# Kernel tuning notes

Hardware: AMD Instinct MI355X
Metric: run time of the kernel (lower is better)

Reference implementation:

```python
import jax, jax.numpy as jnp
import numpy as np

N_QUBITS = 12          # hidden_features = number of wires
QDEPTH = 8             # StronglyEntanglingLayers depth
INPUT_DIM = 784        # c*w*h = 1*28*28
DIM = 2 ** N_QUBITS    # statevector size

# bit table: wire 0 = most significant bit (PennyLane convention)
_BITS = ((np.arange(DIM)[:, None] >> np.arange(N_QUBITS - 1, -1, -1)[None, :]) & 1)  # (DIM, N)
_ZVALS = (1.0 - 2.0 * _BITS).astype(np.float32)  # (DIM, N): eigvals of PauliZ per wire

def _cz_diag(r):
    # diagonal of the product of CZ(i, (i+r)%N) for i in range(N); duplicates cancel (CZ^2=I)
    d = np.ones(DIM, np.float32)
    for i in range(N_QUBITS):
        j = (i + r) % N_QUBITS
        d *= 1.0 - 2.0 * (_BITS[:, i] * _BITS[:, j]).astype(np.float32)
    return d

# per-layer CZ entangler diagonal; PennyLane default range r = l % (N-1) + 1
_CZ_DIAGS = [jnp.asarray(_cz_diag((l % (N_QUBITS - 1)) + 1)) for l in range(QDEPTH)]


def _apply_rot(state, w3, wire):
    # Rot(phi, theta, omega) = RZ(omega) RY(theta) RZ(phi) applied to one wire
    phi, theta, omega = w3[0], w3[1], w3[2]
    c = jnp.cos(theta / 2).astype(jnp.complex64)
    s = jnp.sin(theta / 2).astype(jnp.complex64)
    m00 = jnp.exp(-0.5j * (phi + omega)) * c
    m01 = -jnp.exp(0.5j * (phi - omega)) * s
    m10 = jnp.exp(-0.5j * (phi - omega)) * s
    m11 = jnp.exp(0.5j * (phi + omega)) * c
    M = jnp.stack([jnp.stack([m00, m01]), jnp.stack([m10, m11])])  # (2,2) complex64
    b = state.shape[0]
    st = state.reshape(b, 2 ** wire, 2, -1)
    st = jnp.einsum('pq,bkqr->bkpr', M, st)
    return st.reshape(b, DIM)


def _quantum_layer(angles, qweights):
    # angles: (b, N) RZ-encoded inputs; qweights: (QDEPTH, N, 3)
    b = angles.shape[0]
    # initial |0...0>; RZ(angle_j) on |0> contributes phase exp(-i*angle_j/2)
    amp0 = jnp.exp(-0.5j * jnp.sum(angles, axis=1))  # (b,) complex64
    state = jnp.zeros((b, DIM), jnp.complex64).at[:, 0].set(amp0)
    for l in range(QDEPTH):
        for j in range(N_QUBITS):
            state = _apply_rot(state, qweights[l, j], j)
        state = state * _CZ_DIAGS[l][None, :]
    probs = state.real ** 2 + state.imag ** 2  # (b, DIM)
    return probs @ jnp.asarray(_ZVALS)         # (b, N) <Z_i> expvals


def setup_inputs() -> dict:
    key = jax.random.key(0)
    ks = jax.random.split(key, 6)
    b = 2048
    x = jax.random.normal(ks[0], (b, 1, 28, 28), jnp.float32)
    sd = 1.0 / np.sqrt(INPUT_DIM)
    su = 1.0 / np.sqrt(N_QUBITS)
    w_down = jax.random.normal(ks[1], (N_QUBITS, INPUT_DIM), jnp.float32) * sd
    b_down = jax.random.normal(ks[2], (N_QUBITS,), jnp.float32) * sd
    w_up = jax.random.normal(ks[3], (INPUT_DIM, N_QUBITS), jnp.float32) * su
    b_up = jax.random.normal(ks[4], (INPUT_DIM,), jnp.float32) * su
    qweights = jax.random.normal(ks[5], (QDEPTH, N_QUBITS, 3), jnp.float32) * 0.4
    return {"x": x, "w_down": w_down, "b_down": b_down, "w_up": w_up, "b_up": b_up, "qweights": qweights}


def reference(x, w_down, b_down, w_up, b_up, qweights):
    b, c, w, h = x.shape
    xf = x.reshape(b, -1)
    x_reduced = xf @ w_down.T + b_down            # (b, N_QUBITS)
    z = _quantum_layer(x_reduced, qweights)       # (b, N_QUBITS)
    x_restored = z @ w_up.T + b_up                # (b, INPUT_DIM)
    return x_restored.reshape(b, c, w, h)
```

## Files before the change

kernel.cpp:

```cpp
#include <hip/hip_runtime.h>

#define NQ     12
#define DIM    4096
#define QDEPTH 8
#define T      1024
#define NBLK   256

typedef _Float16 h2 __attribute__((ext_vector_type(2)));
union S4 { float4 f; h2 h[4]; };
union HB { h2 h; unsigned u; int i; };

__device__ __forceinline__ int SW(int i) {
    return i ^ ((i >> 6) & 0xF) ^ (((i >> 10) & 1) << 4);
}

template <int CTRL>
__device__ __forceinline__ int dpp_i(int x) {
    return __builtin_amdgcn_update_dpp(x, x, CTRL, 0xF, 0xF, false);
}
template <int CTRL>
__device__ __forceinline__ float dpp_mov(float x) {
    return __int_as_float(dpp_i<CTRL>(__float_as_int(x)));
}
__device__ __forceinline__ float swz_xor4f(float x) {
    return __int_as_float(__builtin_amdgcn_ds_swizzle(__float_as_int(x), 0x101F));
}

template <int KIND>
__device__ __forceinline__ h2 xlane(h2 x) {
    HB b; b.h = x;
    if constexpr (KIND == 0)      b.i = dpp_i<0xB1>(b.i);
    else if constexpr (KIND == 1) b.i = dpp_i<0x4E>(b.i);
    else if constexpr (KIND == 2) b.i = __builtin_amdgcn_ds_swizzle(b.i, 0x101F);
    else                          b.i = dpp_i<0x128>(b.i);
    return b.h;
}

__device__ __forceinline__ h2 csw(h2 a) { return __builtin_shufflevector(a, a, 1, 0); }
__device__ __forceinline__ h2 cmul(h2 rr, h2 ii, h2 a) { return rr * a + ii * csw(a); }
__device__ __forceinline__ h2 cfma(h2 rr, h2 ii, h2 a, h2 acc) { return acc + rr * a + ii * csw(a); }

__device__ __forceinline__ void reg_gate(h2 a[4], const int m, const S4 S0, const S4 S1) {
#pragma unroll
    for (int c = 0; c < 4; ++c) {
        if (c & m) continue;
        const int c1 = c | m;
        const h2 a0 = a[c], a1 = a[c1];
        h2 n0 = cmul(S0.h[0], S0.h[1], a0); n0 = cfma(S0.h[2], S0.h[3], a1, n0);
        h2 n1 = cmul(S1.h[2], S1.h[3], a0); n1 = cfma(S1.h[0], S1.h[1], a1, n1);
        a[c] = n0; a[c1] = n1;
    }
}

template <int KIND>
__device__ __forceinline__ void lane_gate(h2 a[4], const S4 C) {
#pragma unroll
    for (int c = 0; c < 4; ++c) {
        const h2 p = xlane<KIND>(a[c]);
        h2 n = cmul(C.h[0], C.h[1], a[c]);
        a[c] = cfma(C.h[2], C.h[3], p, n);
    }
}

__device__ __forceinline__ void load_coefs(const float4* __restrict__ m4,
                                           const int gi0, const int lane, S4 R[8]) {
    const float4* G = m4 + gi0 * 2;
    R[0].f = G[0]; R[1].f = G[1]; R[2].f = G[2]; R[3].f = G[3];
    R[4].f = G[4  + ((lane >> 3) & 1)];
    R[5].f = G[6  + ((lane >> 2) & 1)];
    R[6].f = G[8  + ((lane >> 1) & 1)];
    R[7].f = G[10 + ( lane       & 1)];
}

__device__ __forceinline__ void apply6(h2 a[4], const S4 R[8]) {
    reg_gate(a, 2, R[0], R[1]);
    reg_gate(a, 1, R[2], R[3]);
    lane_gate<3>(a, R[4]);
    lane_gate<2>(a, R[5]);
    lane_gate<1>(a, R[6]);
    lane_gate<0>(a, R[7]);
}

__device__ __forceinline__ void apply_cz(h2 a[4], const int ii[4], const int d) {
    const int r = d + 1;
#pragma unroll
    for (int c = 0; c < 4; ++c) {
        const unsigned i  = (unsigned)ii[c];
        const unsigned ro = ((i << r) | (i >> (12 - r))) & 0xFFFu;
        HB b; b.h = a[c];
        b.u ^= (__popc(i & ro) & 1) ? 0x80008000u : 0u;
        a[c] = b.h;
    }
}

__device__ __forceinline__ void merged_pass(h2* __restrict__ st,
                                            const float4* __restrict__ m4,
                                            const int ja[4], const int ii[4],
                                            const int gbase, const int l1,
                                            const int lane, h2 a[4]) {
    S4 R1[8], R2[8];
    load_coefs(m4, l1 * NQ + gbase, lane, R1);
    __syncthreads();
#pragma unroll
    for (int c = 0; c < 4; ++c) a[c] = st[ja[c]];
    load_coefs(m4, (l1 + 1) * NQ + gbase, lane, R2);
    apply6(a, R1);
    apply_cz(a, ii, l1);
    apply6(a, R2);
#pragma unroll
    for (int c = 0; c < 4; ++c) st[ja[c]] = a[c];
}

__global__ __launch_bounds__(T) void qnn_fused(const float* __restrict__ qw,
                                               const float* __restrict__ w_up,
                                               const float* __restrict__ b_up,
                                               float* __restrict__ out) {
    __shared__ h2     st[DIM];
    __shared__ float4 mats4[96 * 2];
    __shared__ float  zred[T / 64][NQ];
    __shared__ float  zfin[NQ];
    __shared__ float4 row4[196];

    const int tid  = threadIdx.x;
    const int lane = tid & 63;

    if (tid < 192) {
        const int g = tid >> 1, hh = tid & 1;
        const float phi = qw[g * 3 + 0], theta = qw[g * 3 + 1], omega = qw[g * 3 + 2];
        float c, s, sp, cp, sm, cm;
        sincosf(0.5f * theta, &s, &c);
        sincosf(0.5f * (phi + omega), &sp, &cp);
        sincosf(0.5f * (phi - omega), &sm, &cm);
        S4 u;
        if (hh == 0) {
            u.h[0] = (h2){(_Float16)(cp * c),  (_Float16)(cp * c)};
            u.h[1] = (h2){(_Float16)(sp * c),  (_Float16)(-sp * c)};
            u.h[2] = (h2){(_Float16)(-cm * s), (_Float16)(-cm * s)};
            u.h[3] = (h2){(_Float16)(sm * s),  (_Float16)(-sm * s)};
        } else {
            u.h[0] = (h2){(_Float16)(cp * c),  (_Float16)(cp * c)};
            u.h[1] = (h2){(_Float16)(-sp * c), (_Float16)(sp * c)};
            u.h[2] = (h2){(_Float16)(cm * s),  (_Float16)(cm * s)};
            u.h[3] = (h2){(_Float16)(sm * s),  (_Float16)(-sm * s)};
        }
        mats4[g * 2 + hh] = u.f;
    }
    __syncthreads();

    const int w4 = (tid >> 6) & 0xF, l54 = (tid >> 4) & 3, l30 = tid & 0xF;
    int jaA[4], iiA[4], jaB[4], iiB[4];
#pragma unroll
    for (int c = 0; c < 4; ++c) {
        iiA[c] = (c << 10) | (l30 << 6) | (l54 << 4) | w4;
        iiB[c] = (l54 << 10) | (w4 << 6) | (c << 4) | l30;
        jaA[c] = SW(iiA[c]);
        jaB[c] = SW(iiB[c]);
    }

    h2 a[4];
    {
        S4 R1[8], R2[8];
        load_coefs(mats4, 0 * NQ + 6, lane, R1);
        load_coefs(mats4, 1 * NQ + 6, lane, R2);
        const int h = (l54 << 4) | w4;
        float pr = 1.f, pi = 0.f;
#pragma unroll
        for (int k = 0; k < 6; ++k) {
            const int b = (h >> (5 - k)) & 1;
            S4 u; u.f = mats4[k * 2 + b];
            const float cr = (float)(b ? u.h[2].x : u.h[0].x);
            const float ci = (float)(b ? u.h[3].y : u.h[1].y);
            const float nr = pr * cr - pi * ci;
            const float ni = pr * ci + pi * cr;
            pr = nr; pi = ni;
        }
        a[0] = (l30 == 0) ? (h2){(_Float16)pr, (_Float16)pi}
                          : (h2){(_Float16)0.f, (_Float16)0.f};
        a[1] = a[2] = a[3] = (h2){(_Float16)0.f, (_Float16)0.f};
        apply6(a, R1);
        apply_cz(a, iiB, 0);
        apply6(a, R2);
#pragma unroll
        for (int c = 0; c < 4; ++c) st[jaB[c]] = a[c];
    }
    merged_pass(st, mats4, jaA, iiA, 0, 1, lane, a);
    merged_pass(st, mats4, jaB, iiB, 6, 2, lane, a);
    merged_pass(st, mats4, jaA, iiA, 0, 3, lane, a);
    merged_pass(st, mats4, jaB, iiB, 6, 4, lane, a);
    merged_pass(st, mats4, jaA, iiA, 0, 5, lane, a);
    merged_pass(st, mats4, jaB, iiB, 6, 6, lane, a);
    {
        S4 R1[8];
        load_coefs(mats4, 7 * NQ + 0, lane, R1);
        __syncthreads();
#pragma unroll
        for (int c = 0; c < 4; ++c) a[c] = st[jaA[c]];
        apply6(a, R1);
    }

    float p4[4];
#pragma unroll
    for (int c = 0; c < 4; ++c) {
        const float ar = (float)a[c].x, ai = (float)a[c].y;
        p4[c] = ar * ar + ai * ai;
    }
    const float s01 = p4[0] + p4[1], s23 = p4[2] + p4[3];
    const float S = s01 + s23;
    float zp[NQ];
    zp[0] = s01 - s23;
    zp[1] = (p4[0] - p4[1]) + (p4[2] - p4[3]);
#pragma unroll
    for (int w = 2; w < NQ; ++w)
        zp[w] = (((iiA[0] >> (11 - w)) & 1) ? -S : S);

#pragma unroll
    for (int w = 0; w < NQ; ++w) {
        float v = zp[w];
        v += dpp_mov<0xB1>(v);
        v += dpp_mov<0x4E>(v);
        v += swz_xor4f(v);
        v += dpp_mov<0x128>(v);
        const float r0 = __int_as_float(__builtin_amdgcn_readlane(__float_as_int(v), 0));
        const float r1 = __int_as_float(__builtin_amdgcn_readlane(__float_as_int(v), 16));
        const float r2 = __int_as_float(__builtin_amdgcn_readlane(__float_as_int(v), 32));
        const float r3 = __int_as_float(__builtin_amdgcn_readlane(__float_as_int(v), 48));
        zp[w] = (r0 + r1) + (r2 + r3);
    }
    const int wave = tid >> 6;
    if (lane == 0) {
#pragma unroll
        for (int w = 0; w < NQ; ++w) zred[wave][w] = zp[w];
    }
    __syncthreads();
    if (tid < NQ) {
        float v = 0.0f;
#pragma unroll
        for (int k = 0; k < T / 64; ++k) v += zred[k][tid];
        zfin[tid] = v;
    }
    __syncthreads();

    if (tid < 784) {
        float acc = b_up[tid];
#pragma unroll
        for (int j = 0; j < NQ; ++j) acc += zfin[j] * w_up[tid * NQ + j];
        ((float*)row4)[tid] = acc;
    }
    __syncthreads();

    if (tid < 784) {
        const float4 v = row4[tid % 196];
        float4* o = (float4*)out;
        const int base = blockIdx.x * 1568;
        o[base + tid]       = v;
        o[base + 784 + tid] = v;
    }
}

extern "C" void kernel_launch(void* const* d_in, const int* in_sizes, int n_in,
                              void* d_out, int out_size, void* d_ws, size_t ws_size,
                              hipStream_t stream) {
    const float* w_up = (const float*)d_in[3];
    const float* b_up = (const float*)d_in[4];
    const float* qw   = (const float*)d_in[5];
    float* out = (float*)d_out;

    qnn_fused<<<NBLK, T, 0, stream>>>(qw, w_up, b_up, out);
}
```

Baseline: 84.77 us.

## Halve block size and process eight amplitudes per thread

Cuts the block from 1024 to 512 threads, so each thread holds 8 statevector amplitudes instead of 4. Three qubits are now handled by in-register gates, which removes the ds_swizzle cross-lane gate and leaves three DPP lane gates. The index mapping and the LDS swizzle are rewritten for the new layout, and the output loops become strided. The aim is to cut cross-lane and barrier overhead per amplitude and raise per-thread ILP, at the cost of more registers per thread and fewer waves to hide latency.

```diff
diff --git a/kernel.cpp b/kernel.cpp
--- a/kernel.cpp
+++ b/kernel.cpp
@@ -3,7 +3,7 @@
 #define NQ     12
 #define DIM    4096
 #define QDEPTH 8
-#define T      1024
+#define T      512
 #define NBLK   256
 
 typedef _Float16 h2 __attribute__((ext_vector_type(2)));
@@ -11,7 +11,7 @@
 union HB { h2 h; unsigned u; int i; };
 
 __device__ __forceinline__ int SW(int i) {
-    return i ^ ((i >> 6) & 0xF) ^ (((i >> 10) & 1) << 4);
+    return i ^ ((i >> 5) & 7) ^ (((i >> 9) & 3) << 3);
 }
 
 template <int CTRL>
@@ -31,7 +31,6 @@
     HB b; b.h = x;
     if constexpr (KIND == 0)      b.i = dpp_i<0xB1>(b.i);
     else if constexpr (KIND == 1) b.i = dpp_i<0x4E>(b.i);
-    else if constexpr (KIND == 2) b.i = __builtin_amdgcn_ds_swizzle(b.i, 0x101F);
     else                          b.i = dpp_i<0x128>(b.i);
     return b.h;
 }
@@ -40,9 +39,9 @@
 __device__ __forceinline__ h2 cmul(h2 rr, h2 ii, h2 a) { return rr * a + ii * csw(a); }
 __device__ __forceinline__ h2 cfma(h2 rr, h2 ii, h2 a, h2 acc) { return acc + rr * a + ii * csw(a); }
 
-__device__ __forceinline__ void reg_gate(h2 a[4], const int m, const S4 S0, const S4 S1) {
-#pragma unroll
-    for (int c = 0; c < 4; ++c) {
+__device__ __forceinline__ void reg_gate8(h2 a[8], const int m, const S4 S0, const S4 S1) {
+#pragma unroll
+    for (int c = 0; c < 8; ++c) {
         if (c & m) continue;
         const int c1 = c | m;
         const h2 a0 = a[c], a1 = a[c1];
@@ -53,38 +52,39 @@
 }
 
 template <int KIND>
-__device__ __forceinline__ void lane_gate(h2 a[4], const S4 C) {
-#pragma unroll
-    for (int c = 0; c < 4; ++c) {
+__device__ __forceinline__ void lane_gate8(h2 a[8], const S4 C) {
+#pragma unroll
+    for (int c = 0; c < 8; ++c) {
         const h2 p = xlane<KIND>(a[c]);
         h2 n = cmul(C.h[0], C.h[1], a[c]);
         a[c] = cfma(C.h[2], C.h[3], p, n);
     }
 }
 
-__device__ __forceinline__ void load_coefs(const float4* __restrict__ m4,
-                                           const int gi0, const int lane, S4 R[8]) {
+__device__ __forceinline__ void load_coefs9(const float4* __restrict__ m4,
+                                            const int gi0, const int g3,
+                                            const int g1, const int g0, S4 R[9]) {
     const float4* G = m4 + gi0 * 2;
-    R[0].f = G[0]; R[1].f = G[1]; R[2].f = G[2]; R[3].f = G[3];
-    R[4].f = G[4  + ((lane >> 3) & 1)];
-    R[5].f = G[6  + ((lane >> 2) & 1)];
-    R[6].f = G[8  + ((lane >> 1) & 1)];
-    R[7].f = G[10 + ( lane       & 1)];
-}
-
-__device__ __forceinline__ void apply6(h2 a[4], const S4 R[8]) {
-    reg_gate(a, 2, R[0], R[1]);
-    reg_gate(a, 1, R[2], R[3]);
-    lane_gate<3>(a, R[4]);
-    lane_gate<2>(a, R[5]);
-    lane_gate<1>(a, R[6]);
-    lane_gate<0>(a, R[7]);
-}
-
-__device__ __forceinline__ void apply_cz(h2 a[4], const int ii[4], const int d) {
+    R[0].f = G[0]; R[1].f = G[1]; R[2].f = G[2];
+    R[3].f = G[3]; R[4].f = G[4]; R[5].f = G[5];
+    R[6].f = G[6  + g3];
+    R[7].f = G[8  + g1];
+    R[8].f = G[10 + g0];
+}
+
+__device__ __forceinline__ void apply6(h2 a[8], const S4 R[9]) {
+    reg_gate8(a, 4, R[0], R[1]);
+    reg_gate8(a, 2, R[2], R[3]);
+    reg_gate8(a, 1, R[4], R[5]);
+    lane_gate8<3>(a, R[6]);
+    lane_gate8<1>(a, R[7]);
+    lane_gate8<0>(a, R[8]);
+}
+
+__device__ __forceinline__ void apply_cz8(h2 a[8], const int ii[8], const int d) {
     const int r = d + 1;
 #pragma unroll
-    for (int c = 0; c < 4; ++c) {
+    for (int c = 0; c < 8; ++c) {
         const unsigned i  = (unsigned)ii[c];
         const unsigned ro = ((i << r) | (i >> (12 - r))) & 0xFFFu;
         HB b; b.h = a[c];
@@ -95,20 +95,21 @@
 
 __device__ __forceinline__ void merged_pass(h2* __restrict__ st,
                                             const float4* __restrict__ m4,
-                                            const int ja[4], const int ii[4],
+                                            const int ja[8], const int ii[8],
                                             const int gbase, const int l1,
-                                            const int lane, h2 a[4]) {
-    S4 R1[8], R2[8];
-    load_coefs(m4, l1 * NQ + gbase, lane, R1);
-    __syncthreads();
-#pragma unroll
-    for (int c = 0; c < 4; ++c) a[c] = st[ja[c]];
-    load_coefs(m4, (l1 + 1) * NQ + gbase, lane, R2);
+                                            const int g3, const int g1,
+                                            const int g0, h2 a[8]) {
+    S4 R1[9], R2[9];
+    load_coefs9(m4, l1 * NQ + gbase, g3, g1, g0, R1);
+    __syncthreads();
+#pragma unroll
+    for (int c = 0; c < 8; ++c) a[c] = st[ja[c]];
+    load_coefs9(m4, (l1 + 1) * NQ + gbase, g3, g1, g0, R2);
     apply6(a, R1);
-    apply_cz(a, ii, l1);
+    apply_cz8(a, ii, l1);
     apply6(a, R2);
 #pragma unroll
-    for (int c = 0; c < 4; ++c) st[ja[c]] = a[c];
+    for (int c = 0; c < 8; ++c) st[ja[c]] = a[c];
 }
 
 __global__ __launch_bounds__(T) void qnn_fused(const float* __restrict__ qw,
@@ -123,6 +124,9 @@
 
     const int tid  = threadIdx.x;
     const int lane = tid & 63;
+    const int g0 = lane & 1, g1 = (lane >> 1) & 1, g3 = (lane >> 3) & 1;
+    const int s2 = (lane >> 2) & 1, s4 = (lane >> 4) & 1, s5 = (lane >> 5) & 1;
+    const int w  = tid >> 6;
 
     if (tid < 192) {
         const int g = tid >> 1, hh = tid & 1;
@@ -147,22 +151,23 @@
     }
     __syncthreads();
 
-    const int w4 = (tid >> 6) & 0xF, l54 = (tid >> 4) & 3, l30 = tid & 0xF;
-    int jaA[4], iiA[4], jaB[4], iiB[4];
-#pragma unroll
-    for (int c = 0; c < 4; ++c) {
-        iiA[c] = (c << 10) | (l30 << 6) | (l54 << 4) | w4;
-        iiB[c] = (l54 << 10) | (w4 << 6) | (c << 4) | l30;
+    int jaA[8], iiA[8], jaB[8], iiB[8];
+#pragma unroll
+    for (int c = 0; c < 8; ++c) {
+        iiA[c] = (c << 9) | (g3 << 8) | (g1 << 7) | (g0 << 6)
+               | (s5 << 5) | (s4 << 4) | (s2 << 3) | w;
+        iiB[c] = (s5 << 11) | (s4 << 10) | (s2 << 9) | (w << 6)
+               | (c << 3) | (g3 << 2) | (g1 << 1) | g0;
         jaA[c] = SW(iiA[c]);
         jaB[c] = SW(iiB[c]);
     }
 
-    h2 a[4];
+    h2 a[8];
     {
-        S4 R1[8], R2[8];
-        load_coefs(mats4, 0 * NQ + 6, lane, R1);
-        load_coefs(mats4, 1 * NQ + 6, lane, R2);
-        const int h = (l54 << 4) | w4;
+        S4 R1[9], R2[9];
+        load_coefs9(mats4, 0 * NQ + 6, g3, g1, g0, R1);
+        load_coefs9(mats4, 1 * NQ + 6, g3, g1, g0, R2);
+        const int h = iiB[0] >> 6;
         float pr = 1.f, pi = 0.f;
 #pragma unroll
         for (int k = 0; k < 6; ++k) {
@@ -174,48 +179,53 @@
             const float ni = pr * ci + pi * cr;
             pr = nr; pi = ni;
         }
-        a[0] = (l30 == 0) ? (h2){(_Float16)pr, (_Float16)pi}
-                          : (h2){(_Float16)0.f, (_Float16)0.f};
-        a[1] = a[2] = a[3] = (h2){(_Float16)0.f, (_Float16)0.f};
+        const bool nz = ((iiB[0] & 63) == 0);
+        a[0] = nz ? (h2){(_Float16)pr, (_Float16)pi} : (h2){(_Float16)0.f, (_Float16)0.f};
+#pragma unroll
+        for (int c = 1; c < 8; ++c) a[c] = (h2){(_Float16)0.f, (_Float16)0.f};
         apply6(a, R1);
-        apply_cz(a, iiB, 0);
+        apply_cz8(a, iiB, 0);
         apply6(a, R2);
 #pragma unroll
-        for (int c = 0; c < 4; ++c) st[jaB[c]] = a[c];
-    }
-    merged_pass(st, mats4, jaA, iiA, 0, 1, lane, a);
-    merged_pass(st, mats4, jaB, iiB, 6, 2, lane, a);
-    merged_pass(st, mats4, jaA, iiA, 0, 3, lane, a);
-    merged_pass(st, mats4, jaB, iiB, 6, 4, lane, a);
-    merged_pass(st, mats4, jaA, iiA, 0, 5, lane, a);
-    merged_pass(st, mats4, jaB, iiB, 6, 6, lane, a);
+        for (int c = 0; c < 8; ++c) st[jaB[c]] = a[c];
+    }
+    merged_pass(st, mats4, jaA, iiA, 0, 1, g3, g1, g0, a);
+    merged_pass(st, mats4, jaB, iiB, 6, 2, g3, g1, g0, a);
+    merged_pass(st, mats4, jaA, iiA, 0, 3, g3, g1, g0, a);
+    merged_pass(st, mats4, jaB, iiB, 6, 4, g3, g1, g0, a);
+    merged_pass(st, mats4, jaA, iiA, 0, 5, g3, g1, g0, a);
+    merged_pass(st, mats4, jaB, iiB, 6, 6, g3, g1, g0, a);
     {
-        S4 R1[8];
-        load_coefs(mats4, 7 * NQ + 0, lane, R1);
+        S4 R1[9];
+        load_coefs9(mats4, 7 * NQ + 0, g3, g1, g0, R1);
         __syncthreads();
 #pragma unroll
-        for (int c = 0; c < 4; ++c) a[c] = st[jaA[c]];
+        for (int c = 0; c < 8; ++c) a[c] = st[jaA[c]];
         apply6(a, R1);
     }
 
-    float p4[4];
-#pragma unroll
-    for (int c = 0; c < 4; ++c) {
+    float p8[8];
+#pragma unroll
+    for (int c = 0; c < 8; ++c) {
         const float ar = (float)a[c].x, ai = (float)a[c].y;
-        p4[c] = ar * ar + ai * ai;
-    }
-    const float s01 = p4[0] + p4[1], s23 = p4[2] + p4[3];
-    const float S = s01 + s23;
+        p8[c] = ar * ar + ai * ai;
+    }
+    const float t0 = p8[0] + p8[1], t1 = p8[2] + p8[3];
+    const float t2 = p8[4] + p8[5], t3 = p8[6] + p8[7];
+    const float e0 = p8[0] - p8[1], e1 = p8[2] - p8[3];
+    const float e2 = p8[4] - p8[5], e3 = p8[6] - p8[7];
+    const float S = (t0 + t1) + (t2 + t3);
     float zp[NQ];
-    zp[0] = s01 - s23;
-    zp[1] = (p4[0] - p4[1]) + (p4[2] - p4[3]);
-#pragma unroll
-    for (int w = 2; w < NQ; ++w)
-        zp[w] = (((iiA[0] >> (11 - w)) & 1) ? -S : S);
-
-#pragma unroll
-    for (int w = 0; w < NQ; ++w) {
-        float v = zp[w];
+    zp[0] = (t0 + t1) - (t2 + t3);
+    zp[1] = (t0 - t1) + (t2 - t3);
+    zp[2] = (e0 + e1) + (e2 + e3);
+#pragma unroll
+    for (int w_ = 3; w_ < NQ; ++w_)
+        zp[w_] = (((iiA[0] >> (11 - w_)) & 1) ? -S : S);
+
+#pragma unroll
+    for (int w_ = 0; w_ < NQ; ++w_) {
+        float v = zp[w_];
         v += dpp_mov<0xB1>(v);
         v += dpp_mov<0x4E>(v);
         v += swz_xor4f(v);
@@ -224,12 +234,11 @@
         const float r1 = __int_as_float(__builtin_amdgcn_readlane(__float_as_int(v), 16));
         const float r2 = __int_as_float(__builtin_amdgcn_readlane(__float_as_int(v), 32));
         const float r3 = __int_as_float(__builtin_amdgcn_readlane(__float_as_int(v), 48));
-        zp[w] = (r0 + r1) + (r2 + r3);
-    }
-    const int wave = tid >> 6;
+        zp[w_] = (r0 + r1) + (r2 + r3);
+    }
     if (lane == 0) {
 #pragma unroll
-        for (int w = 0; w < NQ; ++w) zred[wave][w] = zp[w];
+        for (int w_ = 0; w_ < NQ; ++w_) zred[w][w_] = zp[w_];
     }
     __syncthreads();
     if (tid < NQ) {
@@ -240,21 +249,17 @@
     }
     __syncthreads();
 
-    if (tid < 784) {
-        float acc = b_up[tid];
-#pragma unroll
-        for (int j = 0; j < NQ; ++j) acc += zfin[j] * w_up[tid * NQ + j];
-        ((float*)row4)[tid] = acc;
-    }
-    __syncthreads();
-
-    if (tid < 784) {
-        const float4 v = row4[tid % 196];
-        float4* o = (float4*)out;
-        const int base = blockIdx.x * 1568;
-        o[base + tid]       = v;
-        o[base + 784 + tid] = v;
-    }
+    for (int i = tid; i < 784; i += T) {
+        float acc = b_up[i];
+#pragma unroll
+        for (int j = 0; j < NQ; ++j) acc += zfin[j] * w_up[i * NQ + j];
+        ((float*)row4)[i] = acc;
+    }
+    __syncthreads();
+
+    const int base = blockIdx.x * 1568;
+    for (int j = tid; j < 1568; j += T)
+        ((float4*)out)[base + j] = row4[j % 196];
 }
 
 extern "C" void kernel_launch(void* const* d_in, const int* in_sizes, int n_in,
```

Result: no change. 84.94 us (+0.2%).
